# Kernel tuning notes

Measured on AMD Instinct MI355X. Metric: run time of the kernel, lower is better.

Reference implementation:

```python
import jax, jax.numpy as jnp
import numpy as np

N, E, D = 40000, 320000, 128          # nodes, edges, model dim
H, C = 4, 128                          # GAT heads, per-head channels
DEPTH, MLP = 2, 512
NEG_SLOPE = 0.2
EPS_SM = 1e-16                         # PyG softmax denom epsilon


def layer_norm(x, g, b):
    mu = jnp.mean(x, axis=-1, keepdims=True)
    var = jnp.var(x, axis=-1, keepdims=True)
    return (x - mu) * jax.lax.rsqrt(var + 1e-5) * g + b


def gat_conv(x, src, dst, edge_attr, W, a_src, a_dst, We, a_edge, bias):
    # x: [N,D]; W: [D,H*C]; a_*: [H,C]; We: [1,H*C]; bias: [H*C]
    h = (x @ W).reshape(N, H, C)                       # [N,H,C]
    alpha_src = jnp.einsum('nhc,hc->nh', h, a_src)      # [N,H]
    alpha_dst = jnp.einsum('nhc,hc->nh', h, a_dst)      # [N,H]
    e = (edge_attr @ We).reshape(E, H, C)               # [E,H,C]
    alpha_e = jnp.einsum('ehc,hc->eh', e, a_edge)       # [E,H]
    alpha = alpha_src[src] + alpha_dst[dst] + alpha_e   # [E,H]
    alpha = jax.nn.leaky_relu(alpha, NEG_SLOPE)
    # segment softmax over edges sharing the same destination node
    amax = jax.ops.segment_max(alpha, dst, num_segments=N)   # [N,H]
    ex = jnp.exp(alpha - amax[dst])                          # [E,H]
    denom = jax.ops.segment_sum(ex, dst, num_segments=N)     # [N,H]
    attn = ex / (denom[dst] + EPS_SM)                        # [E,H]
    # message = attn * x_j ; aggregate by destination (scatter-add)
    msg = attn[:, :, None] * h[src]                          # [E,H,C]
    out = jax.ops.segment_sum(msg, dst, num_segments=N)      # [N,H,C]
    return out.reshape(N, H * C) + bias                      # concat heads


def setup_inputs():
    key = jax.random.key(0)
    ks = jax.random.split(key, 16)
    s = 0.05
    f32 = jnp.float32
    inp = {
        'x': jax.random.normal(ks[0], (N, D), f32),
        'edge_index': jax.random.randint(ks[1], (2, E), 0, N),
        'edge_attr': jax.random.normal(ks[2], (E, 1), f32),
        'ln1_g': jnp.ones((DEPTH, D), f32),
        'ln1_b': jnp.zeros((DEPTH, D), f32),
        'gat_W': jax.random.normal(ks[3], (DEPTH, D, H * C), f32) * s,
        'att_src': jax.random.normal(ks[4], (DEPTH, H, C), f32) * s,
        'att_dst': jax.random.normal(ks[5], (DEPTH, H, C), f32) * s,
        'edge_W': jax.random.normal(ks[6], (DEPTH, 1, H * C), f32) * s,
        'att_edge': jax.random.normal(ks[7], (DEPTH, H, C), f32) * s,
        'gat_bias': jnp.zeros((DEPTH, H * C), f32),
        'qf_W': jax.random.normal(ks[8], (DEPTH, H * C, D), f32) * s,
        'qf_b': jnp.zeros((DEPTH, D), f32),
        'ln2_g': jnp.ones((DEPTH, D), f32),
        'ln2_b': jnp.zeros((DEPTH, D), f32),
        'ff_W1': jax.random.normal(ks[9], (DEPTH, D, MLP), f32) * s,
        'ff_b1': jnp.zeros((DEPTH, MLP), f32),
        'ff_W2': jax.random.normal(ks[10], (DEPTH, MLP, D), f32) * s,
        'ff_b2': jnp.zeros((DEPTH, D), f32),
    }
    return inp


def reference(x, edge_index, edge_attr, ln1_g, ln1_b, gat_W, att_src, att_dst,
              edge_W, att_edge, gat_bias, qf_W, qf_b, ln2_g, ln2_b,
              ff_W1, ff_b1, ff_W2, ff_b2):
    src, dst = edge_index[0], edge_index[1]
    for d in range(DEPTH):
        # Residual(PreNorm(QuickFix(GATConv)))
        h = layer_norm(x, ln1_g[d], ln1_b[d])
        g = gat_conv(h, src, dst, edge_attr, gat_W[d], att_src[d], att_dst[d],
                     edge_W[d], att_edge[d], gat_bias[d])
        x = x + g @ qf_W[d] + qf_b[d]
        # Residual(PreNorm(FeedForward))
        h = layer_norm(x, ln2_g[d], ln2_b[d])
        x = x + jax.nn.gelu(h @ ff_W1[d] + ff_b1[d]) @ ff_W2[d] + ff_b2[d]
    return x
```

## Files before the change

kernel.cpp:

```cpp
#include <hip/hip_runtime.h>
#include <hip/hip_bf16.h>

#define N_NODES 40000
#define N_EDGES 320000
#define DIM 128
#define HC 512
#define NHEAD 4
#define CHEAD 128
#define DEPTH_L 2
#define MLP_DIM 512
#define SCAN_NB ((N_NODES + 255) / 256)

typedef __attribute__((ext_vector_type(8))) short short8;
typedef __attribute__((ext_vector_type(4))) float f32x4;

static __device__ __forceinline__ void gload_lds16(const void* g, void* l)
{
    __builtin_amdgcn_global_load_lds(
        (const __attribute__((address_space(1))) unsigned int*)g,
        (__attribute__((address_space(3))) unsigned int*)l,
        16, 0, 0);
}

static __device__ __forceinline__ unsigned int packbf2(float a, float b)
{
    union { __hip_bfloat16 h[2]; unsigned int u; } p;
    p.h[0] = __float2bfloat16(a);
    p.h[1] = __float2bfloat16(b);
    return p.u;
}

static __device__ __forceinline__ float gelu_f(float v)
{
    float z2 = -1.5957691216f * (v + 0.044715f * v * v * v);
    return v / (1.f + __expf(z2));
}

struct PrepArgs {
    const float* wsrc[4];
    __hip_bfloat16* wdst[4];
    int wK[4];
    int wN[4];
    const float* gat_W;
    const float* att_src;
    const float* att_dst;
    const float* edge_W;
    const float* att_edge;
    const float* gat_bias;
    const float* qf_W;
    const float* qf_b;
    float* uvec;
    __hip_bfloat16* Mt;
    float* cvec;
    float* ae;
};
__global__ __launch_bounds__(256) void k_prep(PrepArgs a)
{
    int b = blockIdx.x;
    int tid = threadIdx.x;
    if (b < 1024) {
        int j = b >> 8;
        int i = (b & 255) * 256 + tid;
        int K = a.wK[j], N = a.wN[j];
        if (i < K * N) {
            int n = i / K, k = i % K;
            a.wdst[j][i] = __float2bfloat16(a.wsrc[j][(size_t)k * N + n]);
        }
    } else if (b < 1040) {
        if (tid < 128) {
            int bb = b - 1024;
            int d = bb >> 3, t8 = bb & 7;
            int t = t8 >> 2, h = t8 & 3;
            int c = tid;
            const float* W = a.gat_W + (size_t)d * DIM * HC;
            const float* av = (t == 0 ? a.att_src : a.att_dst)
                              + (size_t)d * NHEAD * CHEAD + h * CHEAD;
            float s = 0.f;
            for (int cc = 0; cc < CHEAD; ++cc)
                s += W[(size_t)c * HC + h * CHEAD + cc] * av[cc];
            a.uvec[(size_t)d * 1024 + t8 * 128 + c] = s;
        }
    } else if (b < 1552) {
        int i = (b - 1040) * 256 + tid;
        int d = i >> 16;
        int hk = (i >> 7) & 511;
        int j = i & 127;
        int h = hk >> 7, k = hk & 127;
        const float* W = a.gat_W + (size_t)d * DIM * HC + (size_t)k * HC + h * CHEAD;
        const float* Q = a.qf_W + (size_t)d * HC * DIM + (size_t)h * CHEAD * DIM + j;
        float s = 0.f;
        for (int c = 0; c < CHEAD; ++c)
            s += W[c] * Q[(size_t)c * DIM];
        a.Mt[(size_t)d * 65536 + (size_t)j * 512 + hk] = __float2bfloat16(s);
    } else if (b < 1616) {
        int idx = (b - 1552) * 4 + (tid >> 6);
        int lane = tid & 63;
        int d = idx >> 7, j = idx & 127;
        float s = 0.f;
        for (int m = lane; m < HC; m += 64)
            s += a.gat_bias[(size_t)d * HC + m]
               * a.qf_W[(size_t)d * HC * DIM + (size_t)m * DIM + j];
        #pragma unroll
        for (int dd = 32; dd; dd >>= 1) s += __shfl_xor(s, dd);
        if (lane == 0) a.cvec[idx] = s + a.qf_b[(size_t)d * DIM + j];
    } else {
        int d = b - 1616;
        int h = tid >> 6, lane = tid & 63;
        float2 w = *reinterpret_cast<const float2*>(
            a.edge_W + (size_t)d * HC + h * CHEAD + lane * 2);
        float2 av = *reinterpret_cast<const float2*>(
            a.att_edge + (size_t)d * NHEAD * CHEAD + h * CHEAD + lane * 2);
        float s = w.x * av.x + w.y * av.y;
        #pragma unroll
        for (int dd = 32; dd; dd >>= 1) s += __shfl_xor(s, dd);
        if (lane == 0) a.ae[d * 4 + h] = s;
    }
}

__global__ void k_hist(const int* __restrict__ dst, int* __restrict__ deg)
{
    int e = blockIdx.x * 256 + threadIdx.x;
    if (e < N_EDGES) atomicAdd(&deg[dst[e]], 1);
}

__global__ __launch_bounds__(256) void k_scan1(const int* __restrict__ deg,
                                               int* __restrict__ off,
                                               int* __restrict__ bsum)
{
    __shared__ int wsum[4];
    int b = blockIdx.x;
    int t = threadIdx.x, lane = t & 63, w = t >> 6;
    int i = b * 256 + t;
    int v = (i < N_NODES) ? deg[i] : 0;
    int s = v;
    #pragma unroll
    for (int d = 1; d < 64; d <<= 1) {
        int u = __shfl_up(s, d);
        if (lane >= d) s += u;
    }
    if (lane == 63) wsum[w] = s;
    __syncthreads();
    int wpre = 0;
    #pragma unroll
    for (int j = 0; j < 4; ++j)
        if (j < w) wpre += wsum[j];
    if (i < N_NODES) off[i] = wpre + s - v;
    if (t == 255) bsum[b] = wpre + s;
}

__global__ __launch_bounds__(256) void k_scan2(int* __restrict__ bsum,
                                               int* __restrict__ bpre)
{
    __shared__ int wsum[4];
    int t = threadIdx.x, lane = t & 63, w = t >> 6;
    int v = (t < SCAN_NB) ? bsum[t] : 0;
    int s = v;
    #pragma unroll
    for (int d = 1; d < 64; d <<= 1) {
        int u = __shfl_up(s, d);
        if (lane >= d) s += u;
    }
    if (lane == 63) wsum[w] = s;
    __syncthreads();
    int wpre = 0;
    #pragma unroll
    for (int j = 0; j < 4; ++j)
        if (j < w) wpre += wsum[j];
    if (t < SCAN_NB) bpre[t] = wpre + s - v;
    if (t == 255) bpre[SCAN_NB] = wpre + s;
}

__global__ __launch_bounds__(256) void k_scan3(int* __restrict__ off,
                                               const int* __restrict__ bpre,
                                               int* __restrict__ cur)
{
    int b = blockIdx.x;
    int i = b * 256 + threadIdx.x;
    if (i < N_NODES) {
        int o = off[i] + bpre[b];
        off[i] = o;
        cur[i] = o;
    }
    if (i == 0) off[N_NODES] = bpre[SCAN_NB];
}

__global__ void k_fill(const int* __restrict__ src, const int* __restrict__ dst,
                       const float* __restrict__ ea, int* __restrict__ cur,
                       int* __restrict__ scsr, int* __restrict__ dcsr,
                       float* __restrict__ eacsr)
{
    int e = blockIdx.x * 256 + threadIdx.x;
    if (e < N_EDGES) {
        int dd = dst[e];
        int p = atomicAdd(&cur[dd], 1);
        scsr[p] = src[e];
        dcsr[p] = dd;
        eacsr[p] = ea[e];
    }
}

__global__ __launch_bounds__(256) void k_ln(const float* __restrict__ x,
                                            const float* __restrict__ gma,
                                            const float* __restrict__ bta,
                                            const float* __restrict__ uvec,
                                            __hip_bfloat16* __restrict__ out,
                                            float* __restrict__ asrc,
                                            float* __restrict__ adst, int M)
{
    int row = blockIdx.x * 4 + (threadIdx.x >> 6);
    int lane = threadIdx.x & 63;
    if (row >= M) return;
    float2 v = *reinterpret_cast<const float2*>(x + (size_t)row * DIM + lane * 2);
    float s = v.x + v.y, sq = v.x * v.x + v.y * v.y;
    #pragma unroll
    for (int d = 32; d; d >>= 1) { s += __shfl_xor(s, d); sq += __shfl_xor(sq, d); }
    float mean = s * (1.f / DIM);
    float var = sq * (1.f / DIM) - mean * mean;
    float rs = rsqrtf(var + 1e-5f);
    int c = lane * 2;
    float h0 = (v.x - mean) * rs * gma[c] + bta[c];
    float h1 = (v.y - mean) * rs * gma[c + 1] + bta[c + 1];
    *reinterpret_cast<unsigned int*>(out + (size_t)row * DIM + c) = packbf2(h0, h1);
    float ss[8];
    #pragma unroll
    for (int tt = 0; tt < 8; ++tt) {
        float2 uv = *reinterpret_cast<const float2*>(uvec + tt * 128 + c);
        ss[tt] = h0 * uv.x + h1 * uv.y;
    }
    #pragma unroll
    for (int d = 32; d; d >>= 1) {
        #pragma unroll
        for (int tt = 0; tt < 8; ++tt) ss[tt] += __shfl_xor(ss[tt], d);
    }
    if (lane == 0) {
        reinterpret_cast<float4*>(asrc)[row] = make_float4(ss[0], ss[1], ss[2], ss[3]);
        reinterpret_cast<float4*>(adst)[row] = make_float4(ss[4], ss[5], ss[6], ss[7]);
    }
}

__global__ __launch_bounds__(256) void k_dots(const unsigned int* __restrict__ hln,
                                              const float* __restrict__ uvec,
                                              float* __restrict__ asrc,
                                              float* __restrict__ adst)
{
    int n = blockIdx.x * 4 + (threadIdx.x >> 6);
    int lane = threadIdx.x & 63;
    unsigned int u = hln[n * 64 + lane];
    float f0 = __uint_as_float(u << 16);
    float f1 = __uint_as_float(u & 0xffff0000u);
    float s[8];
    #pragma unroll
    for (int t = 0; t < 8; ++t) {
        float2 uv = *reinterpret_cast<const float2*>(uvec + t * 128 + lane * 2);
        s[t] = f0 * uv.x + f1 * uv.y;
    }
    #pragma unroll
    for (int d = 32; d; d >>= 1) {
        #pragma unroll
        for (int t = 0; t < 8; ++t) s[t] += __shfl_xor(s[t], d);
    }
    if (lane == 0) {
        reinterpret_cast<float4*>(asrc)[n] = make_float4(s[0], s[1], s[2], s[3]);
        reinterpret_cast<float4*>(adst)[n] = make_float4(s[4], s[5], s[6], s[7]);
    }
}

__global__ __launch_bounds__(256) void k_alpha(const int* __restrict__ scsr,
                                               const int* __restrict__ dcsr,
                                               const float* __restrict__ eacsr,
                                               const float* __restrict__ asrc,
                                               const float* __restrict__ adst,
                                               const float* __restrict__ ae4v,
                                               float* __restrict__ wcsr)
{
    int p = blockIdx.x * 256 + threadIdx.x;
    if (p >= N_EDGES) return;
    int s = scsr[p], dd = dcsr[p];
    float q = eacsr[p];
    float4 as = reinterpret_cast<const float4*>(asrc)[s];
    float4 ad = reinterpret_cast<const float4*>(adst)[dd];
    float4 ae = *reinterpret_cast<const float4*>(ae4v);
    float4 w;
    float al;
    al = as.x + ad.x + ae.x * q; al = al > 0.f ? al : 0.2f * al; w.x = __expf(al);
    al = as.y + ad.y + ae.y * q; al = al > 0.f ? al : 0.2f * al; w.y = __expf(al);
    al = as.z + ad.z + ae.z * q; al = al > 0.f ? al : 0.2f * al; w.z = __expf(al);
    al = as.w + ad.w + ae.w * q; al = al > 0.f ? al : 0.2f * al; w.w = __expf(al);
    reinterpret_cast<float4*>(wcsr)[p] = w;
}

__global__ __launch_bounds__(256) void k_agg2(const int* __restrict__ off,
                                              const int* __restrict__ scsr,
                                              const float* __restrict__ wcsr,
                                              const unsigned int* __restrict__ hln,
                                              unsigned int* __restrict__ agg)
{
    int n = blockIdx.x * 4 + (threadIdx.x >> 6);
    int lane = threadIdx.x & 63;
    int e0 = off[n], e1 = off[n + 1];
    float den[4] = {0, 0, 0, 0};
    float accA[4] = {0, 0, 0, 0};
    float accB[4] = {0, 0, 0, 0};
    int i = e0;
    for (; i + 1 < e1; i += 2) {
        int s0 = scsr[i], s1 = scsr[i + 1];
        float4 w0 = reinterpret_cast<const float4*>(wcsr)[i];
        float4 w1 = reinterpret_cast<const float4*>(wcsr)[i + 1];
        unsigned int u0 = hln[s0 * 64 + lane];
        unsigned int u1 = hln[s1 * 64 + lane];
        float f00 = __uint_as_float(u0 << 16);
        float f01 = __uint_as_float(u0 & 0xffff0000u);
        float f10 = __uint_as_float(u1 << 16);
        float f11 = __uint_as_float(u1 & 0xffff0000u);
        den[0] += w0.x + w1.x; den[1] += w0.y + w1.y;
        den[2] += w0.z + w1.z; den[3] += w0.w + w1.w;
        accA[0] += w0.x * f00 + w1.x * f10; accB[0] += w0.x * f01 + w1.x * f11;
        accA[1] += w0.y * f00 + w1.y * f10; accB[1] += w0.y * f01 + w1.y * f11;
        accA[2] += w0.z * f00 + w1.z * f10; accB[2] += w0.z * f01 + w1.z * f11;
        accA[3] += w0.w * f00 + w1.w * f10; accB[3] += w0.w * f01 + w1.w * f11;
    }
    if (i < e1) {
        int s0 = scsr[i];
        float4 w0 = reinterpret_cast<const float4*>(wcsr)[i];
        unsigned int u0 = hln[s0 * 64 + lane];
        float f00 = __uint_as_float(u0 << 16);
        float f01 = __uint_as_float(u0 & 0xffff0000u);
        den[0] += w0.x; den[1] += w0.y; den[2] += w0.z; den[3] += w0.w;
        accA[0] += w0.x * f00; accB[0] += w0.x * f01;
        accA[1] += w0.y * f00; accB[1] += w0.y * f01;
        accA[2] += w0.z * f00; accB[2] += w0.z * f01;
        accA[3] += w0.w * f00; accB[3] += w0.w * f01;
    }
    #pragma unroll
    for (int h = 0; h < 4; ++h) {
        float inv = 1.f / (den[h] + 1e-16f);
        agg[n * 256 + h * 64 + lane] = packbf2(accA[h] * inv, accB[h] * inv);
    }
}

template <bool LN>
__global__ __launch_bounds__(256) void k_qf(const short* __restrict__ A,
                                            const short* __restrict__ Bt,
                                            const float* __restrict__ bias,
                                            const float* __restrict__ resid,
                                            float* __restrict__ xout,
                                            const float* __restrict__ gma,
                                            const float* __restrict__ bta,
                                            __hip_bfloat16* __restrict__ hout,
                                            int M)
{
    __shared__ __align__(16) short Bls[2][128 * 64];
    const int tid = threadIdx.x;
    const int lane = tid & 63;
    const int w = tid >> 6;
    const int lrow = lane & 15;
    const int lk = lane >> 4;
    const int mw = blockIdx.x * 64 + w * 16;

    short8 aq[16];
    #pragma unroll
    for (int t = 0; t < 16; ++t)
        aq[t] = *reinterpret_cast<const short8*>(
            A + (size_t)(mw + lrow) * 512 + t * 32 + lk * 8);

    auto stage = [&](int buf, int kt) {
        #pragma unroll
        for (int c0 = 0; c0 < 1024; c0 += 256) {
            int c = c0 + tid;
            int wb = c0 + (w << 6);
            int r = c >> 3, gq = c & 7, gp = gq ^ (r & 7);
            gload_lds16(Bt + (size_t)r * 512 + kt + gp * 8, &Bls[buf][wb * 8]);
        }
    };

    f32x4 acc[8] = {};
    stage(0, 0);
    __syncthreads();
    int cur = 0;
    for (int t = 0; t < 8; ++t) {
        if (t < 7) stage(cur ^ 1, (t + 1) * 64);
        #pragma unroll
        for (int ks = 0; ks < 2; ++ks) {
            short8 af = aq[t * 2 + ks];
            short8 bf[8];
            #pragma unroll
            for (int fj = 0; fj < 8; ++fj) {
                int r = fj * 16 + lrow;
                int g = ks * 4 + lk;
                bf[fj] = *reinterpret_cast<const short8*>(
                    &Bls[cur][r * 64 + ((g ^ (r & 7)) * 8)]);
            }
            #pragma unroll
            for (int fj = 0; fj < 8; ++fj)
                acc[fj] = __builtin_amdgcn_mfma_f32_16x16x32_bf16(
                    af, bf[fj], acc[fj], 0, 0, 0);
        }
        __syncthreads();
        cur ^= 1;
    }

    #pragma unroll
    for (int p = 0; p < 4; ++p) {
        int m = mw + lk * 4 + p;
        float v[8], s = 0.f, sq = 0.f;
        #pragma unroll
        for (int fj = 0; fj < 8; ++fj) {
            int n = fj * 16 + lrow;
            v[fj] = acc[fj][p] + bias[n] + resid[(size_t)m * DIM + n];
            s += v[fj]; sq += v[fj] * v[fj];
        }
        #pragma unroll
        for (int fj = 0; fj < 8; ++fj)
            xout[(size_t)m * DIM + fj * 16 + lrow] = v[fj];
        if (LN) {
            #pragma unroll
            for (int d = 1; d < 16; d <<= 1) {
                s += __shfl_xor(s, d);
                sq += __shfl_xor(sq, d);
            }
            float mean = s * (1.f / DIM);
            float var = sq * (1.f / DIM) - mean * mean;
            float rs = rsqrtf(var + 1e-5f);
            #pragma unroll
            for (int fj = 0; fj < 8; ++fj) {
                int n = fj * 16 + lrow;
                hout[(size_t)m * DIM + n] =
                    __float2bfloat16((v[fj] - mean) * rs * gma[n] + bta[n]);
            }
        }
    }
}

template <bool LNN>
__global__ __launch_bounds__(256) void k_ff(const short* __restrict__ A,
                                            const short* __restrict__ W1t,
                                            const short* __restrict__ W2t,
                                            const float* __restrict__ b1,
                                            const float* __restrict__ b2,
                                            const float* __restrict__ resid,
                                            float* __restrict__ xout,
                                            const float* __restrict__ gma,
                                            const float* __restrict__ bta,
                                            __hip_bfloat16* __restrict__ hout,
                                            int M)
{
    __shared__ __align__(16) short B1ls[64 * 128];
    __shared__ __align__(16) short B2ls[128 * 64];
    __shared__ __align__(16) short midls[4][16 * 64];
    const int tid = threadIdx.x;
    const int lane = tid & 63;
    const int w = tid >> 6;
    const int lrow = lane & 15;
    const int lk = lane >> 4;
    const int mw = blockIdx.x * 64 + w * 16;
    __hip_bfloat16* midw = (__hip_bfloat16*)midls[w];

    short8 af[4];
    #pragma unroll
    for (int ks = 0; ks < 4; ++ks)
        af[ks] = *reinterpret_cast<const short8*>(
            A + (size_t)(mw + lrow) * 128 + ks * 32 + lk * 8);

    auto stage1 = [&](int mc) {
        #pragma unroll
        for (int c0 = 0; c0 < 1024; c0 += 256) {
            int c = c0 + tid;
            int wb = c0 + (w << 6);
            int r = c >> 4, gq = c & 15, gp = gq ^ (r & 15);
            gload_lds16(W1t + (size_t)(mc * 64 + r) * 128 + gp * 8, &B1ls[wb * 8]);
        }
    };
    auto stage2 = [&](int mc) {
        #pragma unroll
        for (int c0 = 0; c0 < 1024; c0 += 256) {
            int c = c0 + tid;
            int wb = c0 + (w << 6);
            int r = c >> 3, gq = c & 7, gp = gq ^ (r & 7);
            gload_lds16(W2t + (size_t)r * 512 + mc * 64 + gp * 8, &B2ls[wb * 8]);
        }
    };

    f32x4 acc2[8] = {};
    stage1(0);
    for (int mc = 0; mc < 8; ++mc) {
        __syncthreads();
        stage2(mc);
        f32x4 acc1[4] = {};
        #pragma unroll
        for (int ks = 0; ks < 4; ++ks) {
            short8 bf1[4];
            #pragma unroll
            for (int fj = 0; fj < 4; ++fj) {
                int r = fj * 16 + lrow;
                bf1[fj] = *reinterpret_cast<const short8*>(
                    &B1ls[r * 128 + (((ks * 4 + lk) ^ (r & 15)) * 8)]);
            }
            #pragma unroll
            for (int fj = 0; fj < 4; ++fj)
                acc1[fj] = __builtin_amdgcn_mfma_f32_16x16x32_bf16(
                    af[ks], bf1[fj], acc1[fj], 0, 0, 0);
        }
        #pragma unroll
        for (int fj = 0; fj < 4; ++fj) {
            #pragma unroll
            for (int p = 0; p < 4; ++p) {
                int mloc = lk * 4 + p;
                int cloc = fj * 16 + lrow;
                float v = gelu_f(acc1[fj][p] + b1[mc * 64 + cloc]);
                int slot = (cloc >> 3) ^ (mloc & 7);
                midw[mloc * 64 + slot * 8 + (cloc & 7)] = __float2bfloat16(v);
            }
        }
        __syncthreads();
        if (mc < 7) stage1(mc + 1);
        #pragma unroll
        for (int ks2 = 0; ks2 < 2; ++ks2) {
            int g = ks2 * 4 + lk;
            short8 a2 = *reinterpret_cast<const short8*>(
                &midls[w][lrow * 64 + ((g ^ (lrow & 7)) * 8)]);
            short8 bf2[8];
            #pragma unroll
            for (int fj = 0; fj < 8; ++fj) {
                int r = fj * 16 + lrow;
                bf2[fj] = *reinterpret_cast<const short8*>(
                    &B2ls[r * 64 + ((g ^ (r & 7)) * 8)]);
            }
            #pragma unroll
            for (int fj = 0; fj < 8; ++fj)
                acc2[fj] = __builtin_amdgcn_mfma_f32_16x16x32_bf16(
                    a2, bf2[fj], acc2[fj], 0, 0, 0);
        }
    }

    #pragma unroll
    for (int p = 0; p < 4; ++p) {
        int m = mw + lk * 4 + p;
        float v[8], s = 0.f, sq = 0.f;
        #pragma unroll
        for (int fj = 0; fj < 8; ++fj) {
            int n = fj * 16 + lrow;
            v[fj] = acc2[fj][p] + b2[n] + resid[(size_t)m * DIM + n];
            s += v[fj]; sq += v[fj] * v[fj];
        }
        #pragma unroll
        for (int fj = 0; fj < 8; ++fj)
            xout[(size_t)m * DIM + fj * 16 + lrow] = v[fj];
        if (LNN) {
            #pragma unroll
            for (int d = 1; d < 16; d <<= 1) {
                s += __shfl_xor(s, d);
                sq += __shfl_xor(sq, d);
            }
            float mean = s * (1.f / DIM);
            float var = sq * (1.f / DIM) - mean * mean;
            float rs = rsqrtf(var + 1e-5f);
            #pragma unroll
            for (int fj = 0; fj < 8; ++fj) {
                int n = fj * 16 + lrow;
                hout[(size_t)m * DIM + n] =
                    __float2bfloat16((v[fj] - mean) * rs * gma[n] + bta[n]);
            }
        }
    }
}

extern "C" void kernel_launch(void* const* d_in, const int* in_sizes, int n_in,
                              void* d_out, int out_size, void* d_ws, size_t ws_size,
                              hipStream_t stream)
{
    const float* x_in     = (const float*)d_in[0];
    const int*   ei       = (const int*)d_in[1];
    const float* ea       = (const float*)d_in[2];
    const float* ln1_g    = (const float*)d_in[3];
    const float* ln1_b    = (const float*)d_in[4];
    const float* gat_W    = (const float*)d_in[5];
    const float* att_src  = (const float*)d_in[6];
    const float* att_dst  = (const float*)d_in[7];
    const float* edge_W   = (const float*)d_in[8];
    const float* att_edge = (const float*)d_in[9];
    const float* gat_bias = (const float*)d_in[10];
    const float* qf_W     = (const float*)d_in[11];
    const float* qf_b     = (const float*)d_in[12];
    const float* ln2_g    = (const float*)d_in[13];
    const float* ln2_b    = (const float*)d_in[14];
    const float* ff_W1    = (const float*)d_in[15];
    const float* ff_b1    = (const float*)d_in[16];
    const float* ff_W2    = (const float*)d_in[17];
    const float* ff_b2    = (const float*)d_in[18];
    float* x = (float*)d_out;

    char* ws = (char*)d_ws;
    size_t o = 0;
    auto alloc = [&](size_t b) { size_t r = o; o += (b + 255) & ~(size_t)255; return r; };
    __hip_bfloat16*  h_ln  = (__hip_bfloat16*)(ws + alloc((size_t)N_NODES * DIM * 2));
    __hip_bfloat16*  gbuf  = (__hip_bfloat16*)(ws + alloc((size_t)N_NODES * HC * 2));
    float*           asrc  = (float*)(ws + alloc((size_t)N_NODES * 4 * 4));
    float*           adst  = (float*)(ws + alloc((size_t)N_NODES * 4 * 4));
    float*           ae4   = (float*)(ws + alloc(256));
    float*           uvec  = (float*)(ws + alloc((size_t)DEPTH_L * 1024 * 4));
    __hip_bfloat16*  Mt    = (__hip_bfloat16*)(ws + alloc((size_t)DEPTH_L * 65536 * 2));
    float*           cvec  = (float*)(ws + alloc(256 * 4));
    int*             deg   = (int*)(ws + alloc((size_t)(N_NODES + 1) * 4));
    int*             off   = (int*)(ws + alloc((size_t)(N_NODES + 1) * 4));
    int*             cur   = (int*)(ws + alloc((size_t)N_NODES * 4));
    int*             bsum  = (int*)(ws + alloc((size_t)(SCAN_NB + 1) * 4));
    int*             bpre  = (int*)(ws + alloc((size_t)(SCAN_NB + 1) * 4));
    int*             scsr  = (int*)(ws + alloc((size_t)N_EDGES * 4));
    int*             dcsr  = (int*)(ws + alloc((size_t)N_EDGES * 4));
    float*           eacsr = (float*)(ws + alloc((size_t)N_EDGES * 4));
    float*           wcsr  = (float*)(ws + alloc((size_t)N_EDGES * 4 * 4));
    __hip_bfloat16* Wt[DEPTH_L][2];
    for (int d = 0; d < DEPTH_L; ++d)
        for (int j = 0; j < 2; ++j)
            Wt[d][j] = (__hip_bfloat16*)(ws + alloc((size_t)65536 * 2));

    const int* srcA = ei;
    const int* dstA = ei + N_EDGES;

    PrepArgs pa;
    for (int d = 0; d < DEPTH_L; ++d) {
        pa.wsrc[d * 2 + 0] = ff_W1 + (size_t)d * DIM * MLP_DIM;
        pa.wK[d * 2 + 0] = DIM;     pa.wN[d * 2 + 0] = MLP_DIM;
        pa.wsrc[d * 2 + 1] = ff_W2 + (size_t)d * MLP_DIM * DIM;
        pa.wK[d * 2 + 1] = MLP_DIM; pa.wN[d * 2 + 1] = DIM;
        pa.wdst[d * 2 + 0] = Wt[d][0];
        pa.wdst[d * 2 + 1] = Wt[d][1];
    }
    pa.gat_W = gat_W; pa.att_src = att_src; pa.att_dst = att_dst;
    pa.edge_W = edge_W; pa.att_edge = att_edge;
    pa.gat_bias = gat_bias; pa.qf_W = qf_W; pa.qf_b = qf_b;
    pa.uvec = uvec; pa.Mt = Mt; pa.cvec = cvec; pa.ae = ae4;
    k_prep<<<1618, 256, 0, stream>>>(pa);

    hipMemsetAsync(deg, 0, (size_t)(N_NODES + 1) * 4, stream);
    k_hist<<<(N_EDGES + 255) / 256, 256, 0, stream>>>(dstA, deg);
    k_scan1<<<SCAN_NB, 256, 0, stream>>>(deg, off, bsum);
    k_scan2<<<1, 256, 0, stream>>>(bsum, bpre);
    k_scan3<<<SCAN_NB, 256, 0, stream>>>(off, bpre, cur);
    k_fill<<<(N_EDGES + 255) / 256, 256, 0, stream>>>(srcA, dstA, ea, cur, scsr, dcsr, eacsr);

    const int QB = N_NODES / 64;
    const int NB = N_NODES / 4;
    const int EB = (N_EDGES + 255) / 256;

    k_ln<<<NB, 256, 0, stream>>>(x_in, ln1_g, ln1_b, uvec, h_ln, asrc, adst, N_NODES);

    for (int d = 0; d < DEPTH_L; ++d) {
        const float* resid0 = (d == 0) ? x_in : x;
        k_alpha<<<EB, 256, 0, stream>>>(scsr, dcsr, eacsr, asrc, adst, ae4 + d * 4, wcsr);
        k_agg2<<<NB, 256, 0, stream>>>(off, scsr, wcsr, (const unsigned int*)h_ln,
            (unsigned int*)gbuf);
        k_qf<true><<<QB, 256, 0, stream>>>((const short*)gbuf,
            (const short*)(Mt + (size_t)d * 65536), cvec + d * 128, resid0, x,
            ln2_g + d * DIM, ln2_b + d * DIM, h_ln, N_NODES);
        if (d + 1 < DEPTH_L) {
            k_ff<true><<<QB, 256, 0, stream>>>((const short*)h_ln,
                (const short*)Wt[d][0], (const short*)Wt[d][1],
                ff_b1 + d * MLP_DIM, ff_b2 + d * DIM, x, x,
                ln1_g + (d + 1) * DIM, ln1_b + (d + 1) * DIM, h_ln, N_NODES);
            k_dots<<<NB, 256, 0, stream>>>((const unsigned int*)h_ln,
                uvec + (size_t)(d + 1) * 1024, asrc, adst);
        } else {
            k_ff<false><<<QB, 256, 0, stream>>>((const short*)h_ln,
                (const short*)Wt[d][0], (const short*)Wt[d][1],
                ff_b1 + d * MLP_DIM, ff_b2 + d * DIM, x, x,
                nullptr, nullptr, nullptr, N_NODES);
        }
    }
}
```

Measured before the change: 278.7 us.

## Split wavefront into four edge groups with 16-byte gathers in GAT aggregation

The aggregation kernel now splits each 64-lane wavefront into four 16-lane groups, each handling a different incoming edge per iteration and loading 8 bf16 features per lane as a uint4. Partial sums for all 4 heads x 8 channels are combined across groups with xor shuffles, and the first group writes the normalized result with 16-byte stores. The aim is more independent edges in flight and wider memory transactions for the irregular row gathers. In exchange each lane holds 32 accumulators, the shuffle reduction adds cross-lane work, and lanes idle when a node's edge count is not a multiple of four.

```diff
diff --git a/kernel.cpp b/kernel.cpp
--- a/kernel.cpp
+++ b/kernel.cpp
@@ -292,49 +292,59 @@
 __global__ __launch_bounds__(256) void k_agg2(const int* __restrict__ off,
                                               const int* __restrict__ scsr,
                                               const float* __restrict__ wcsr,
-                                              const unsigned int* __restrict__ hln,
-                                              unsigned int* __restrict__ agg)
+                                              const uint4* __restrict__ hln4,
+                                              uint4* __restrict__ agg4)
 {
     int n = blockIdx.x * 4 + (threadIdx.x >> 6);
     int lane = threadIdx.x & 63;
+    int g = lane >> 4;
+    int lg = lane & 15;
     int e0 = off[n], e1 = off[n + 1];
     float den[4] = {0, 0, 0, 0};
-    float accA[4] = {0, 0, 0, 0};
-    float accB[4] = {0, 0, 0, 0};
-    int i = e0;
-    for (; i + 1 < e1; i += 2) {
-        int s0 = scsr[i], s1 = scsr[i + 1];
-        float4 w0 = reinterpret_cast<const float4*>(wcsr)[i];
-        float4 w1 = reinterpret_cast<const float4*>(wcsr)[i + 1];
-        unsigned int u0 = hln[s0 * 64 + lane];
-        unsigned int u1 = hln[s1 * 64 + lane];
-        float f00 = __uint_as_float(u0 << 16);
-        float f01 = __uint_as_float(u0 & 0xffff0000u);
-        float f10 = __uint_as_float(u1 << 16);
-        float f11 = __uint_as_float(u1 & 0xffff0000u);
-        den[0] += w0.x + w1.x; den[1] += w0.y + w1.y;
-        den[2] += w0.z + w1.z; den[3] += w0.w + w1.w;
-        accA[0] += w0.x * f00 + w1.x * f10; accB[0] += w0.x * f01 + w1.x * f11;
-        accA[1] += w0.y * f00 + w1.y * f10; accB[1] += w0.y * f01 + w1.y * f11;
-        accA[2] += w0.z * f00 + w1.z * f10; accB[2] += w0.z * f01 + w1.z * f11;
-        accA[3] += w0.w * f00 + w1.w * f10; accB[3] += w0.w * f01 + w1.w * f11;
-    }
-    if (i < e1) {
-        int s0 = scsr[i];
-        float4 w0 = reinterpret_cast<const float4*>(wcsr)[i];
-        unsigned int u0 = hln[s0 * 64 + lane];
-        float f00 = __uint_as_float(u0 << 16);
-        float f01 = __uint_as_float(u0 & 0xffff0000u);
-        den[0] += w0.x; den[1] += w0.y; den[2] += w0.z; den[3] += w0.w;
-        accA[0] += w0.x * f00; accB[0] += w0.x * f01;
-        accA[1] += w0.y * f00; accB[1] += w0.y * f01;
-        accA[2] += w0.z * f00; accB[2] += w0.z * f01;
-        accA[3] += w0.w * f00; accB[3] += w0.w * f01;
-    }
-    #pragma unroll
-    for (int h = 0; h < 4; ++h) {
-        float inv = 1.f / (den[h] + 1e-16f);
-        agg[n * 256 + h * 64 + lane] = packbf2(accA[h] * inv, accB[h] * inv);
+    float acc[4][8] = {};
+    for (int i = e0; i < e1; i += 4) {
+        int ii = i + g;
+        bool valid = ii < e1;
+        int idx = valid ? ii : e0;
+        int s0 = scsr[idx];
+        float4 w = reinterpret_cast<const float4*>(wcsr)[idx];
+        if (!valid) { w.x = 0.f; w.y = 0.f; w.z = 0.f; w.w = 0.f; }
+        uint4 v = hln4[(size_t)s0 * 16 + lg];
+        float f[8];
+        f[0] = __uint_as_float(v.x << 16); f[1] = __uint_as_float(v.x & 0xffff0000u);
+        f[2] = __uint_as_float(v.y << 16); f[3] = __uint_as_float(v.y & 0xffff0000u);
+        f[4] = __uint_as_float(v.z << 16); f[5] = __uint_as_float(v.z & 0xffff0000u);
+        f[6] = __uint_as_float(v.w << 16); f[7] = __uint_as_float(v.w & 0xffff0000u);
+        den[0] += w.x; den[1] += w.y; den[2] += w.z; den[3] += w.w;
+        #pragma unroll
+        for (int c = 0; c < 8; ++c) {
+            acc[0][c] += w.x * f[c];
+            acc[1][c] += w.y * f[c];
+            acc[2][c] += w.z * f[c];
+            acc[3][c] += w.w * f[c];
+        }
+    }
+    #pragma unroll
+    for (int d = 16; d < 64; d <<= 1) {
+        #pragma unroll
+        for (int h = 0; h < 4; ++h) {
+            den[h] += __shfl_xor(den[h], d);
+            #pragma unroll
+            for (int c = 0; c < 8; ++c)
+                acc[h][c] += __shfl_xor(acc[h][c], d);
+        }
+    }
+    if (g == 0) {
+        #pragma unroll
+        for (int h = 0; h < 4; ++h) {
+            float inv = 1.f / (den[h] + 1e-16f);
+            uint4 o;
+            o.x = packbf2(acc[h][0] * inv, acc[h][1] * inv);
+            o.y = packbf2(acc[h][2] * inv, acc[h][3] * inv);
+            o.z = packbf2(acc[h][4] * inv, acc[h][5] * inv);
+            o.w = packbf2(acc[h][6] * inv, acc[h][7] * inv);
+            agg4[(size_t)n * 64 + h * 16 + lg] = o;
+        }
     }
 }
 
@@ -648,8 +658,8 @@
     for (int d = 0; d < DEPTH_L; ++d) {
         const float* resid0 = (d == 0) ? x_in : x;
         k_alpha<<<EB, 256, 0, stream>>>(scsr, dcsr, eacsr, asrc, adst, ae4 + d * 4, wcsr);
-        k_agg2<<<NB, 256, 0, stream>>>(off, scsr, wcsr, (const unsigned int*)h_ln,
-            (unsigned int*)gbuf);
+        k_agg2<<<NB, 256, 0, stream>>>(off, scsr, wcsr, (const uint4*)h_ln,
+            (uint4*)gbuf);
         k_qf<true><<<QB, 256, 0, stream>>>((const short*)gbuf,
             (const short*)(Mt + (size_t)d * 65536), cvec + d * 128, resid0, x,
             ln2_g + d * DIM, ln2_b + d * DIM, h_ln, N_NODES);
```

New measurement: 289.0 us. 1.04x slower.

## Fuse attention dot products into FF epilogue and unroll aggregation by four

Applied to the files above, without the earlier changes.

Drops the separate k_dots kernel. The next layer's source and destination attention scores are now computed inside the k_ff LayerNorm epilogue, using fp32 normalized values and a 16-lane shuffle reduction. This avoids re-reading h_ln and one kernel launch. The aggregation loop is also unrolled from two to four edges per iteration to keep more gathers in flight, at the cost of higher register pressure in both kernels (64 extra uvec registers in k_ff).

```diff
diff --git a/kernel.cpp b/kernel.cpp
--- a/kernel.cpp
+++ b/kernel.cpp
@@ -238,33 +238,6 @@
     }
 }
 
-__global__ __launch_bounds__(256) void k_dots(const unsigned int* __restrict__ hln,
-                                              const float* __restrict__ uvec,
-                                              float* __restrict__ asrc,
-                                              float* __restrict__ adst)
-{
-    int n = blockIdx.x * 4 + (threadIdx.x >> 6);
-    int lane = threadIdx.x & 63;
-    unsigned int u = hln[n * 64 + lane];
-    float f0 = __uint_as_float(u << 16);
-    float f1 = __uint_as_float(u & 0xffff0000u);
-    float s[8];
-    #pragma unroll
-    for (int t = 0; t < 8; ++t) {
-        float2 uv = *reinterpret_cast<const float2*>(uvec + t * 128 + lane * 2);
-        s[t] = f0 * uv.x + f1 * uv.y;
-    }
-    #pragma unroll
-    for (int d = 32; d; d >>= 1) {
-        #pragma unroll
-        for (int t = 0; t < 8; ++t) s[t] += __shfl_xor(s[t], d);
-    }
-    if (lane == 0) {
-        reinterpret_cast<float4*>(asrc)[n] = make_float4(s[0], s[1], s[2], s[3]);
-        reinterpret_cast<float4*>(adst)[n] = make_float4(s[4], s[5], s[6], s[7]);
-    }
-}
-
 __global__ __launch_bounds__(256) void k_alpha(const int* __restrict__ scsr,
                                                const int* __restrict__ dcsr,
                                                const float* __restrict__ eacsr,
@@ -302,24 +275,34 @@
     float accA[4] = {0, 0, 0, 0};
     float accB[4] = {0, 0, 0, 0};
     int i = e0;
-    for (; i + 1 < e1; i += 2) {
-        int s0 = scsr[i], s1 = scsr[i + 1];
+    for (; i + 3 < e1; i += 4) {
+        int s0 = scsr[i], s1 = scsr[i + 1], s2 = scsr[i + 2], s3 = scsr[i + 3];
         float4 w0 = reinterpret_cast<const float4*>(wcsr)[i];
         float4 w1 = reinterpret_cast<const float4*>(wcsr)[i + 1];
+        float4 w2 = reinterpret_cast<const float4*>(wcsr)[i + 2];
+        float4 w3 = reinterpret_cast<const float4*>(wcsr)[i + 3];
         unsigned int u0 = hln[s0 * 64 + lane];
         unsigned int u1 = hln[s1 * 64 + lane];
-        float f00 = __uint_as_float(u0 << 16);
-        float f01 = __uint_as_float(u0 & 0xffff0000u);
-        float f10 = __uint_as_float(u1 << 16);
-        float f11 = __uint_as_float(u1 & 0xffff0000u);
-        den[0] += w0.x + w1.x; den[1] += w0.y + w1.y;
-        den[2] += w0.z + w1.z; den[3] += w0.w + w1.w;
-        accA[0] += w0.x * f00 + w1.x * f10; accB[0] += w0.x * f01 + w1.x * f11;
-        accA[1] += w0.y * f00 + w1.y * f10; accB[1] += w0.y * f01 + w1.y * f11;
-        accA[2] += w0.z * f00 + w1.z * f10; accB[2] += w0.z * f01 + w1.z * f11;
-        accA[3] += w0.w * f00 + w1.w * f10; accB[3] += w0.w * f01 + w1.w * f11;
-    }
-    if (i < e1) {
+        unsigned int u2 = hln[s2 * 64 + lane];
+        unsigned int u3 = hln[s3 * 64 + lane];
+        float f00 = __uint_as_float(u0 << 16), f01 = __uint_as_float(u0 & 0xffff0000u);
+        float f10 = __uint_as_float(u1 << 16), f11 = __uint_as_float(u1 & 0xffff0000u);
+        float f20 = __uint_as_float(u2 << 16), f21 = __uint_as_float(u2 & 0xffff0000u);
+        float f30 = __uint_as_float(u3 << 16), f31 = __uint_as_float(u3 & 0xffff0000u);
+        den[0] += (w0.x + w1.x) + (w2.x + w3.x);
+        den[1] += (w0.y + w1.y) + (w2.y + w3.y);
+        den[2] += (w0.z + w1.z) + (w2.z + w3.z);
+        den[3] += (w0.w + w1.w) + (w2.w + w3.w);
+        accA[0] += w0.x * f00 + w1.x * f10 + w2.x * f20 + w3.x * f30;
+        accB[0] += w0.x * f01 + w1.x * f11 + w2.x * f21 + w3.x * f31;
+        accA[1] += w0.y * f00 + w1.y * f10 + w2.y * f20 + w3.y * f30;
+        accB[1] += w0.y * f01 + w1.y * f11 + w2.y * f21 + w3.y * f31;
+        accA[2] += w0.z * f00 + w1.z * f10 + w2.z * f20 + w3.z * f30;
+        accB[2] += w0.z * f01 + w1.z * f11 + w2.z * f21 + w3.z * f31;
+        accA[3] += w0.w * f00 + w1.w * f10 + w2.w * f20 + w3.w * f30;
+        accB[3] += w0.w * f01 + w1.w * f11 + w2.w * f21 + w3.w * f31;
+    }
+    for (; i < e1; ++i) {
         int s0 = scsr[i];
         float4 w0 = reinterpret_cast<const float4*>(wcsr)[i];
         unsigned int u0 = hln[s0 * 64 + lane];
@@ -442,6 +425,9 @@
                                             const float* __restrict__ gma,
                                             const float* __restrict__ bta,
                                             __hip_bfloat16* __restrict__ hout,
+                                            const float* __restrict__ uvec,
+                                            float* __restrict__ asrcO,
+                                            float* __restrict__ adstO,
                                             int M)
 {
     __shared__ __align__(16) short B1ls[64 * 128];
@@ -532,6 +518,15 @@
         }
     }
 
+    float uvv[8][8];
+    if (LNN) {
+        #pragma unroll
+        for (int tt = 0; tt < 8; ++tt)
+            #pragma unroll
+            for (int fj = 0; fj < 8; ++fj)
+                uvv[tt][fj] = uvec[tt * 128 + fj * 16 + lrow];
+    }
+
     #pragma unroll
     for (int p = 0; p < 4; ++p) {
         int m = mw + lk * 4 + p;
@@ -554,11 +549,25 @@
             float mean = s * (1.f / DIM);
             float var = sq * (1.f / DIM) - mean * mean;
             float rs = rsqrtf(var + 1e-5f);
+            float ss[8] = {0, 0, 0, 0, 0, 0, 0, 0};
             #pragma unroll
             for (int fj = 0; fj < 8; ++fj) {
                 int n = fj * 16 + lrow;
-                hout[(size_t)m * DIM + n] =
-                    __float2bfloat16((v[fj] - mean) * rs * gma[n] + bta[n]);
+                float h = (v[fj] - mean) * rs * gma[n] + bta[n];
+                hout[(size_t)m * DIM + n] = __float2bfloat16(h);
+                #pragma unroll
+                for (int tt = 0; tt < 8; ++tt) ss[tt] += h * uvv[tt][fj];
+            }
+            #pragma unroll
+            for (int d = 1; d < 16; d <<= 1) {
+                #pragma unroll
+                for (int tt = 0; tt < 8; ++tt) ss[tt] += __shfl_xor(ss[tt], d);
+            }
+            if (lrow == 0) {
+                reinterpret_cast<float4*>(asrcO)[m] =
+                    make_float4(ss[0], ss[1], ss[2], ss[3]);
+                reinterpret_cast<float4*>(adstO)[m] =
+                    make_float4(ss[4], ss[5], ss[6], ss[7]);
             }
         }
     }
@@ -657,13 +666,13 @@
             k_ff<true><<<QB, 256, 0, stream>>>((const short*)h_ln,
                 (const short*)Wt[d][0], (const short*)Wt[d][1],
                 ff_b1 + d * MLP_DIM, ff_b2 + d * DIM, x, x,
-                ln1_g + (d + 1) * DIM, ln1_b + (d + 1) * DIM, h_ln, N_NODES);
-            k_dots<<<NB, 256, 0, stream>>>((const unsigned int*)h_ln,
-                uvec + (size_t)(d + 1) * 1024, asrc, adst);
+                ln1_g + (d + 1) * DIM, ln1_b + (d + 1) * DIM, h_ln,
+                uvec + (size_t)(d + 1) * 1024, asrc, adst, N_NODES);
         } else {
             k_ff<false><<<QB, 256, 0, stream>>>((const short*)h_ln,
                 (const short*)Wt[d][0], (const short*)Wt[d][1],
                 ff_b1 + d * MLP_DIM, ff_b2 + d * DIM, x, x,
+                nullptr, nullptr, nullptr,
                 nullptr, nullptr, nullptr, N_NODES);
         }
     }
```

Result: faster. 261.8 us, median of 2 (-6.1%).
